# Kernel tuning notes

Measured on AMD Instinct MI355X. Metric: run time of the kernel, lower is better.

The kernel has to match this reference:

```python
import jax, jax.numpy as jnp
import numpy as np

B, S, D, H, T = 64, 512, 768, 384, 22  # batch, seq, bert dim, lstm hidden, tagset+2


def setup_inputs() -> dict:
    key = jax.random.key(0)
    ks = jax.random.split(key, 14)
    hidden_states = jax.random.normal(ks[0], (B, S, D), jnp.float32)
    # strictly increasing wordpiece start offsets, -1 padded (per-sample variable length)
    nw = np.array([S // 2 - (b % 16) * 4 for b in range(B)])  # number of valid start ids
    sid = -np.ones((B, S), np.int64)
    msk = np.zeros((B, S), np.int64)
    for b in range(B):
        sid[b, : nw[b]] = 1 + 2 * np.arange(nw[b])  # max = 2*nw-1 <= S-1
        msk[b, : nw[b] + 1] = 1  # word-level mask: nw+1 words incl. CLS slot
    start_ids = jnp.asarray(sid)
    masks = jnp.asarray(msk)
    sc = 0.05
    h0 = jax.random.normal(ks[1], (2, B, H), jnp.float32)
    c0 = jax.random.normal(ks[2], (2, B, H), jnp.float32)
    W_ih_f = jax.random.normal(ks[3], (4 * H, D), jnp.float32) * sc
    W_hh_f = jax.random.normal(ks[4], (4 * H, H), jnp.float32) * sc
    b_ih_f = jax.random.normal(ks[5], (4 * H,), jnp.float32) * sc
    b_hh_f = jax.random.normal(ks[6], (4 * H,), jnp.float32) * sc
    W_ih_b = jax.random.normal(ks[7], (4 * H, D), jnp.float32) * sc
    W_hh_b = jax.random.normal(ks[8], (4 * H, H), jnp.float32) * sc
    b_ih_b = jax.random.normal(ks[9], (4 * H,), jnp.float32) * sc
    b_hh_b = jax.random.normal(ks[10], (4 * H,), jnp.float32) * sc
    W_lin = jax.random.normal(ks[11], (T, 2 * H), jnp.float32) * sc
    b_lin = jax.random.normal(ks[12], (T,), jnp.float32) * sc
    return {"hidden_states": hidden_states, "h0": h0, "c0": c0,
            "W_ih_f": W_ih_f, "W_hh_f": W_hh_f, "b_ih_f": b_ih_f, "b_hh_f": b_hh_f,
            "W_ih_b": W_ih_b, "W_hh_b": W_hh_b, "b_ih_b": b_ih_b, "b_hh_b": b_hh_b,
            "W_lin": W_lin, "b_lin": b_lin, "start_ids": start_ids, "masks": masks}


def _lstm_dir(x, h0, c0, Wih, Whh, bih, bhh, reverse):
    # x: [B,S,D]; torch gate order i,f,g,o
    xg = jnp.einsum('bsd,gd->bsg', x, Wih) + bih + bhh  # [B,S,4H]
    xs = jnp.swapaxes(xg, 0, 1)  # [S,B,4H]
    if reverse:
        xs = xs[::-1]

    def step(carry, xt):
        h, c = carry
        g = xt + h @ Whh.T
        i, f, gg, o = jnp.split(g, 4, axis=-1)
        c = jax.nn.sigmoid(f) * c + jax.nn.sigmoid(i) * jnp.tanh(gg)
        h = jax.nn.sigmoid(o) * jnp.tanh(c)
        return (h, c), h

    _, hs = jax.lax.scan(step, (h0, c0), xs)
    if reverse:
        hs = hs[::-1]
    return jnp.swapaxes(hs, 0, 1)  # [B,S,H]


def _align(hidden_states, start_ids, masks):
    # word t embedding: t==0 -> token 0 (CLS); 1<=t<n -> token start_ids[t]-1
    # (last wordpiece of word t); t==n -> token start_ids[n-1]; else zero-pad.
    Bb, Ss, _ = hidden_states.shape
    t = jnp.arange(Ss)[None, :]
    valid = start_ids >= 0
    n = valid.sum(-1)  # [B] number of valid start ids
    last_sid = jnp.take_along_axis(start_ids, (n - 1)[:, None], axis=1)  # [B,1]
    idx = jnp.where(t == 0, 0,
          jnp.where(t < n[:, None], start_ids - 1,
          jnp.where(t == n[:, None], last_sid, 0)))
    idx = jnp.clip(idx, 0, Ss - 1)
    gathered = jnp.take_along_axis(hidden_states, idx[:, :, None], axis=1)
    sent_len = masks.sum(-1)  # word-level lengths (second loop in torch code)
    keep = (t < sent_len[:, None])[:, :, None]
    return jnp.where(keep, gathered, 0.0)


def reference(hidden_states, h0, c0, W_ih_f, W_hh_f, b_ih_f, b_hh_f,
              W_ih_b, W_hh_b, b_ih_b, b_hh_b, W_lin, b_lin, start_ids, masks):
    embeds = _align(hidden_states, start_ids, masks)  # q=1,k=0 => wordpiece-only
    hf = _lstm_dir(embeds, h0[0], c0[0], W_ih_f, W_hh_f, b_ih_f, b_hh_f, False)
    hb = _lstm_dir(embeds, h0[1], c0[1], W_ih_b, W_hh_b, b_ih_b, b_hh_b, True)
    lstm_out = jnp.concatenate([hf, hb], axis=-1)  # [B,S,2H]
    # dropout1 is identity in eval mode
    feats = lstm_out @ W_lin.T + b_lin  # [B,S,T]
    return feats
```

## Files before the change

### kernel.cpp

```cpp
#include <hip/hip_runtime.h>

typedef unsigned short u16;
typedef unsigned int u32;
typedef unsigned long long u64;

typedef short bf16x8 __attribute__((ext_vector_type(8)));
typedef float f32x4 __attribute__((ext_vector_type(4)));
typedef u32 u32x4 __attribute__((ext_vector_type(4)));

#define NB 64
#define NS 512
#define ND 768
#define NH 384
#define NT_OUT 22
#define S2 272
#define NG 1536
#define MGEMM (NB*S2)
#define MAGIC 0x5A5AA5A5u
#define MAX_RETRY 1000000

__device__ __forceinline__ u16 f2b(float f) {
    u32 u = __float_as_uint(f);
    u32 r = (u + 0x7fffu + ((u >> 16) & 1u)) >> 16;
    return (u16)r;
}
__device__ __forceinline__ float b2f(u16 s) { return __uint_as_float(((u32)s) << 16); }

__device__ __forceinline__ float sigm(float x) {
    return __builtin_amdgcn_rcpf(1.f + __expf(-x));
}
__device__ __forceinline__ float tanh_(float x) {
    return 1.f - 2.f * __builtin_amdgcn_rcpf(1.f + __expf(2.f * x));
}

__device__ __forceinline__ void gl_lds16(const void* g, void* l) {
    __builtin_amdgcn_global_load_lds(
        (const __attribute__((address_space(1))) unsigned int*)g,
        (__attribute__((address_space(3))) unsigned int*)l, 16, 0, 0);
}

__device__ __forceinline__ u32 ld_sc0(const int* p) {
    u32 v;
    asm volatile("global_load_dword %0, %1, off sc0 nt\n\t"
                 "s_waitcnt vmcnt(0)"
                 : "=&v"(v) : "v"(p) : "memory");
    return v;
}
__device__ __forceinline__ void st_sc0(int* p, u32 v) {
    asm volatile("global_store_dword %0, %1, off sc0" :: "v"(p), "v"(v) : "memory");
}

__device__ __forceinline__ void ld6_fast_nw(const u32* p,
        u32x4& A, u32x4& B, u32x4& C, u32x4& D, u32x4& E, u32x4& F) {
    asm volatile(
        "global_load_dwordx4 %0, %6, off sc0 nt\n\t"
        "global_load_dwordx4 %1, %6, off offset:16 sc0 nt\n\t"
        "global_load_dwordx4 %2, %6, off offset:128 sc0 nt\n\t"
        "global_load_dwordx4 %3, %6, off offset:144 sc0 nt\n\t"
        "global_load_dwordx4 %4, %6, off offset:256 sc0 nt\n\t"
        "global_load_dwordx4 %5, %6, off offset:272 sc0 nt"
        : "=&v"(A), "=&v"(B), "=&v"(C), "=&v"(D), "=&v"(E), "=&v"(F)
        : "v"(p) : "memory");
}
__device__ __forceinline__ void ld6_fast_wt(const u32* p,
        u32x4& A, u32x4& B, u32x4& C, u32x4& D, u32x4& E, u32x4& F) {
    asm volatile(
        "global_load_dwordx4 %0, %6, off sc0 nt\n\t"
        "global_load_dwordx4 %1, %6, off offset:16 sc0 nt\n\t"
        "global_load_dwordx4 %2, %6, off offset:128 sc0 nt\n\t"
        "global_load_dwordx4 %3, %6, off offset:144 sc0 nt\n\t"
        "global_load_dwordx4 %4, %6, off offset:256 sc0 nt\n\t"
        "global_load_dwordx4 %5, %6, off offset:272 sc0 nt\n\t"
        "s_waitcnt vmcnt(0)"
        : "=&v"(A), "=&v"(B), "=&v"(C), "=&v"(D), "=&v"(E), "=&v"(F)
        : "v"(p) : "memory");
}
__device__ __forceinline__ void ld6_slow(const u32* p,
        u32x4& A, u32x4& B, u32x4& C, u32x4& D, u32x4& E, u32x4& F) {
    #pragma unroll
    for (int e = 0; e < 4; e++) {
        A[e] = __hip_atomic_load(p + e,      __ATOMIC_RELAXED, __HIP_MEMORY_SCOPE_AGENT);
        B[e] = __hip_atomic_load(p + 4 + e,  __ATOMIC_RELAXED, __HIP_MEMORY_SCOPE_AGENT);
        C[e] = __hip_atomic_load(p + 32 + e, __ATOMIC_RELAXED, __HIP_MEMORY_SCOPE_AGENT);
        D[e] = __hip_atomic_load(p + 36 + e, __ATOMIC_RELAXED, __HIP_MEMORY_SCOPE_AGENT);
        E[e] = __hip_atomic_load(p + 64 + e, __ATOMIC_RELAXED, __HIP_MEMORY_SCOPE_AGENT);
        F[e] = __hip_atomic_load(p + 68 + e, __ATOMIC_RELAXED, __HIP_MEMORY_SCOPE_AGENT);
    }
}
__device__ __forceinline__ void ld6_nw(bool fast, const u32* p,
        u32x4& A, u32x4& B, u32x4& C, u32x4& D, u32x4& E, u32x4& F) {
    if (fast) ld6_fast_nw(p, A, B, C, D, E, F);
    else      ld6_slow(p, A, B, C, D, E, F);
}
__device__ __forceinline__ void ld6_wt(bool fast, const u32* p,
        u32x4& A, u32x4& B, u32x4& C, u32x4& D, u32x4& E, u32x4& F) {
    if (fast) ld6_fast_wt(p, A, B, C, D, E, F);
    else      ld6_slow(p, A, B, C, D, E, F);
}
__device__ __forceinline__ void st8(bool fast, u32* p, u32x4 lo, u32x4 hi) {
    if (fast)
        asm volatile("global_store_dwordx4 %0, %1, off sc0\n\t"
                     "global_store_dwordx4 %0, %2, off offset:16 sc0"
                     :: "v"(p), "v"(lo), "v"(hi) : "memory");
    else {
        #pragma unroll
        for (int e = 0; e < 4; e++) {
            __hip_atomic_store(p + e,     lo[e], __ATOMIC_RELAXED, __HIP_MEMORY_SCOPE_AGENT);
            __hip_atomic_store(p + 4 + e, hi[e], __ATOMIC_RELAXED, __HIP_MEMORY_SCOPE_AGENT);
        }
    }
}
__device__ __forceinline__ void wait_vm6() {
    __builtin_amdgcn_sched_barrier(0);
    asm volatile("s_waitcnt vmcnt(6)" ::: "memory");
    __builtin_amdgcn_sched_barrier(0);
}
__device__ __forceinline__ void wait_vm0() {
    __builtin_amdgcn_sched_barrier(0);
    asm volatile("s_waitcnt vmcnt(0)" ::: "memory");
    __builtin_amdgcn_sched_barrier(0);
}
__device__ __forceinline__ void ldsbar() {
    asm volatile("s_waitcnt lgkmcnt(0)" ::: "memory");
    __builtin_amdgcn_s_barrier();
    __builtin_amdgcn_sched_barrier(0);
}

__device__ __forceinline__ u32 sum6(const u32x4& a, const u32x4& b, const u32x4& c,
                                    const u32x4& d, const u32x4& e, const u32x4& f) {
    u32 s = (a[0] & 0xffffu) + (a[1] & 0xffffu) + (a[2] & 0xffffu) + (a[3] & 0xffffu);
    s += (b[0] & 0xffffu) + (b[1] & 0xffffu) + (b[2] & 0xffffu) + (b[3] & 0xffffu);
    s += (c[0] & 0xffffu) + (c[1] & 0xffffu) + (c[2] & 0xffffu) + (c[3] & 0xffffu);
    s += (d[0] & 0xffffu) + (d[1] & 0xffffu) + (d[2] & 0xffffu) + (d[3] & 0xffffu);
    s += (e[0] & 0xffffu) + (e[1] & 0xffffu) + (e[2] & 0xffffu) + (e[3] & 0xffffu);
    s += (f[0] & 0xffffu) + (f[1] & 0xffffu) + (f[2] & 0xffffu) + (f[3] & 0xffffu);
    return s;
}
__device__ __forceinline__ bf16x8 packf(const u32x4& lo, const u32x4& hi) {
    union { u32 q[4]; bf16x8 v; } U;
    U.q[0] = __builtin_amdgcn_perm(lo[1], lo[0], 0x07060302u);
    U.q[1] = __builtin_amdgcn_perm(lo[3], lo[2], 0x07060302u);
    U.q[2] = __builtin_amdgcn_perm(hi[1], hi[0], 0x07060302u);
    U.q[3] = __builtin_amdgcn_perm(hi[3], hi[2], 0x07060302u);
    return U.v;
}

__global__ void k_prep(const float* __restrict__ hidden, const int* __restrict__ start_ids,
                       const int* __restrict__ masks, u16* __restrict__ embeds) {
    int b = blockIdx.x >> 2;
    int quarter = blockIdx.x & 3;
    int tid = threadIdx.x;
    __shared__ int red[256];
    int cn = 0, cm = 0;
    for (int s = tid; s < NS; s += 256) {
        cn += (start_ids[b * NS + s] >= 0) ? 1 : 0;
        cm += (masks[b * NS + s] != 0) ? 1 : 0;
    }
    red[tid] = cn + (cm << 16);
    __syncthreads();
    #pragma unroll
    for (int off = 128; off > 0; off >>= 1) {
        if (tid < off) red[tid] += red[tid + off];
        __syncthreads();
    }
    int n = red[0] & 0xffff;
    int slen = red[0] >> 16;
    n = min(max(n, 1), NS);
    int last = start_ids[b * NS + n - 1];
    for (int t = quarter * 68; t < quarter * 68 + 68; ++t) {
        int idx;
        if (t == 0) idx = 0;
        else if (t < n) idx = start_ids[b * NS + t] - 1;
        else if (t == n) idx = last;
        else idx = 0;
        idx = min(max(idx, 0), NS - 1);
        bool keep = t < slen;
        const float* src = hidden + ((size_t)b * NS + idx) * ND;
        u16* dst = embeds + ((size_t)b * S2 + t) * ND;
        if (tid < 192) {
            float4 v = keep ? *(const float4*)(src + tid * 4) : make_float4(0.f, 0.f, 0.f, 0.f);
            union { u16 u[4]; uint2 q; } pk;
            pk.u[0] = f2b(v.x); pk.u[1] = f2b(v.y); pk.u[2] = f2b(v.z); pk.u[3] = f2b(v.w);
            *(uint2*)(dst + tid * 4) = pk.q;
        }
    }
}

__global__ void k_weights(const float* __restrict__ wf, const float* __restrict__ wb,
                          const float* __restrict__ bihf, const float* __restrict__ bhhf,
                          const float* __restrict__ bihb, const float* __restrict__ bhhb,
                          const float* __restrict__ h0,
                          u16* __restrict__ wihcat, float* __restrict__ biascat,
                          u16* __restrict__ h0buf) {
    int i0 = blockIdx.x * blockDim.x + threadIdx.x;
    int NTH = gridDim.x * blockDim.x;
    for (size_t i = i0; i < (size_t)2 * NG * ND; i += NTH) {
        size_t nrow = i / ND, k = i - nrow * ND;
        float v = (nrow < NG) ? wf[nrow * ND + k] : wb[(nrow - NG) * ND + k];
        wihcat[i] = f2b(v);
    }
    for (int i = i0; i < 2 * NG; i += NTH)
        biascat[i] = (i < NG) ? bihf[i] + bhhf[i] : bihb[i - NG] + bhhb[i - NG];
    for (int i = i0; i < 2 * NB * NH; i += NTH) h0buf[i] = f2b(h0[i]);
}

__global__ void k_packwhh(const float* __restrict__ whhf, const float* __restrict__ whhb,
                          u16* __restrict__ pack) {
    int ft = blockIdx.x * 256 + threadIdx.x;
    if (ft >= 2 * 4 * 4 * 6 * 12 * 64) return;
    int lane = ft & 63;
    int grp = ft >> 6;
    int ks = grp % 12; grp /= 12;
    int nt = grp % 6;  grp /= 6;
    int w  = grp & 3;  grp >>= 2;
    int qc = grp & 3;
    int d  = grp >> 2;
    const float* W = d ? whhb : whhf;
    int col = w * NH + qc * 96 + nt * 16 + (lane & 15);
    int k0 = ks * 32 + (lane >> 4) * 8;
    u16* dst = pack + (size_t)ft * 8;
    #pragma unroll
    for (int e = 0; e < 8; e++) dst[e] = f2b(W[(size_t)col * NH + k0 + e]);
}

__launch_bounds__(256, 2)
__global__ void k_gemm(const u16* __restrict__ A, const u16* __restrict__ Bw,
                       const float* __restrict__ biascat, u16* __restrict__ xg) {
    __shared__ u16 As[128 * 32];
    __shared__ u16 Bs[128 * 32];
    int tid = threadIdx.x;
    int lane = tid & 63, wid = tid >> 6;
    int l15 = lane & 15, q4 = lane >> 4;
    int bn = blockIdx.x;
    int bm = blockIdx.y;
    int wm = (wid >> 1) * 64, wn = (wid & 1) * 64;
    f32x4 acc[4][4] = {};
    for (int k0 = 0; k0 < ND; k0 += 32) {
        #pragma unroll
        for (int j = 0; j < 2; j++) {
            int fl = tid + j * 256;
            int row = fl >> 2, cb = fl & 3;
            const u16* ga = A + (size_t)(bm * 128 + row) * ND + k0 + cb * 8;
            gl_lds16(ga, &As[(size_t)(wid * 64 + j * 256) * 8]);
            const u16* gb = Bw + (size_t)(bn * 128 + row) * ND + k0 + cb * 8;
            gl_lds16(gb, &Bs[(size_t)(wid * 64 + j * 256) * 8]);
        }
        __syncthreads();
        bf16x8 af[4], bf[4];
        #pragma unroll
        for (int mt = 0; mt < 4; mt++)
            af[mt] = *(const bf16x8*)&As[(wm + mt * 16 + l15) * 32 + q4 * 8];
        #pragma unroll
        for (int nt = 0; nt < 4; nt++)
            bf[nt] = *(const bf16x8*)&Bs[(wn + nt * 16 + l15) * 32 + q4 * 8];
        #pragma unroll
        for (int mt = 0; mt < 4; mt++)
            #pragma unroll
            for (int nt = 0; nt < 4; nt++)
                acc[mt][nt] = __builtin_amdgcn_mfma_f32_16x16x32_bf16(af[mt], bf[nt], acc[mt][nt], 0, 0, 0);
        __syncthreads();
    }
    #pragma unroll
    for (int nt = 0; nt < 4; nt++) {
        int gn = bn * 128 + wn + nt * 16 + l15;
        int d = gn >= NG ? 1 : 0;
        int col = gn - d * NG;
        float bias = biascat[gn];
        #pragma unroll
        for (int mt = 0; mt < 4; mt++) {
            #pragma unroll
            for (int r = 0; r < 4; r++) {
                int m = bm * 128 + wm + mt * 16 + q4 * 4 + r;
                int b = m / S2, t = m - b * S2;
                float v = acc[mt][nt][r] + bias;
                xg[((size_t)(d * NB + b) * S2 + t) * NG + col] = f2b(v);
            }
        }
    }
}

__launch_bounds__(256, 1)
__global__ void k_recur(const u16* __restrict__ whhpack, const u16* __restrict__ xg,
                        const float* __restrict__ biascat, const u16* __restrict__ h0buf,
                        const float* __restrict__ c0, u16* __restrict__ hout,
                        int* __restrict__ flags, u32* __restrict__ xch) {
    const int blk = blockIdx.x;
    const int qc = blk >> 3;
    const int cl = blk & 7;
    const int d = cl >> 2;
    const int g = cl & 3;
    const int tid = threadIdx.x, lane = tid & 63, w = tid >> 6;
    const int q4 = lane >> 4, l15 = lane & 15;

    __shared__ float preact[4][16 * 96];
    __shared__ u16 hlds[16 * 104];
    __shared__ int s_fast;

    bf16x8 bfr[6][12];
    #pragma unroll
    for (int nt = 0; nt < 6; nt++)
        #pragma unroll
        for (int j = 0; j < 12; j++) {
            int ksg = ((qc + (j / 3)) & 3) * 3 + (j % 3);
            bfr[nt][j] = *(const bf16x8*)(whhpack +
                ((size_t)((((d * 4 + qc) * 4 + w) * 6 + nt) * 12 + ksg) * 64 + lane) * 8);
        }

    const int bb = tid / 12;
    const int j0 = (tid % 12) * 8;
    float cre[8];
    if (tid < 192) {
        const float* cp = c0 + (size_t)(d * NB + g * 16 + bb) * NH + qc * 96 + j0;
        #pragma unroll
        for (int e = 0; e < 8; e++) cre[e] = cp[e];
    }
    float biasreg[6];
    #pragma unroll
    for (int nt = 0; nt < 6; nt++)
        biasreg[nt] = biascat[d * NG + w * NH + qc * 96 + nt * 16 + l15];

    if (tid == 0) {
        int* pzb = flags + cl * 64;
        int* pmb = flags + 2048 + cl * 64;
        st_sc0(pzb + qc * 16, MAGIC);
        u32 seen = 1u << qc;
        for (int spin = 0; spin < 512 && seen != 0xFu; ++spin) {
            #pragma unroll
            for (int r = 0; r < 4; ++r)
                if (!((seen >> r) & 1u) && ld_sc0(pzb + r * 16) == MAGIC) seen |= 1u << r;
            __builtin_amdgcn_s_sleep(2);
        }
        __hip_atomic_store(pmb + qc * 16, (int)(0x100u | seen),
                           __ATOMIC_RELAXED, __HIP_MEMORY_SCOPE_AGENT);
        u32 m = 0xFu;
        int spin2 = 0;
        #pragma unroll
        for (int r = 0; r < 4; ++r) {
            u32 v;
            do {
                v = (u32)__hip_atomic_load(pmb + r * 16, __ATOMIC_RELAXED,
                                           __HIP_MEMORY_SCOPE_AGENT);
            } while (!(v & 0x100u) && ++spin2 < MAX_RETRY);
            m &= v;
        }
        s_fast = ((m & 0xFu) == 0xFu && spin2 < MAX_RETRY) ? 1 : 0;
    }
    __syncthreads();
    const bool fast = (s_fast != 0);

    const u16* xgd = xg + (size_t)d * NB * S2 * NG;

    float ci[6][4];
    auto preload = [&](int it2) {
        int s2 = d ? (NS - 1 - it2) : it2;
        if (s2 < S2) {
            const u16* xrow = xgd + ((size_t)(g * 16) * S2 + s2) * NG + w * NH + qc * 96 + l15;
            #pragma unroll
            for (int nt = 0; nt < 6; nt++)
                #pragma unroll
                for (int r = 0; r < 4; r++)
                    ci[nt][r] = b2f(xrow[(size_t)(q4 * 4 + r) * S2 * NG + nt * 16]);
        } else {
            #pragma unroll
            for (int nt = 0; nt < 6; nt++)
                #pragma unroll
                for (int r = 0; r < 4; r++) ci[nt][r] = biasreg[nt];
        }
    };
    preload(0);

    #pragma unroll 1
    for (int it = 0; it < NS; ++it) {
        int s = d ? (NS - 1 - it) : it;
        f32x4 acc[6];

        if (it == 0) {
            bf16x8 af0[12];
            const u16* hp = h0buf + (size_t)(d * NB + g * 16) * NH;
            #pragma unroll
            for (int j = 0; j < 12; j++) {
                int ksg = ((qc + (j / 3)) & 3) * 3 + (j % 3);
                af0[j] = *(const bf16x8*)(hp + (size_t)l15 * NH + ksg * 32 + q4 * 8);
            }
            #pragma unroll
            for (int nt = 0; nt < 6; nt++) {
                acc[nt][0] = ci[nt][0]; acc[nt][1] = ci[nt][1];
                acc[nt][2] = ci[nt][2]; acc[nt][3] = ci[nt][3];
            }
            preload(1);
            #pragma unroll
            for (int j = 0; j < 12; j++)
                #pragma unroll
                for (int nt = 0; nt < 6; nt++)
                    acc[nt] = __builtin_amdgcn_mfma_f32_16x16x32_bf16(af0[j], bfr[nt][j], acc[nt], 0, 0, 0);
        } else {
            bf16x8 afo0 = *(const bf16x8*)&hlds[l15 * 104 + 0 * 32 + q4 * 8];
            bf16x8 afo1 = *(const bf16x8*)&hlds[l15 * 104 + 1 * 32 + q4 * 8];
            bf16x8 afo2 = *(const bf16x8*)&hlds[l15 * 104 + 2 * 32 + q4 * 8];
            const u32 T = (u32)it;
            const u32 want = T * 24u;
            u32* xrow = xch + (((size_t)(T & 3u) * 8 + cl) * 16 + l15) * 384 + q4 * 8;
            u32* pA = xrow + ((qc + 1) & 3) * 96;
            u32* pB = xrow + ((qc + 2) & 3) * 96;
            u32* pC = xrow + ((qc + 3) & 3) * 96;
            u32x4 a0, a1, a2, a3, a4, a5, b0, b1, b2, b3, b4, b5, e0, e1, e2, e3, e4, e5;
            ld6_nw(fast, pA, a0, a1, a2, a3, a4, a5);
            ld6_nw(fast, pB, b0, b1, b2, b3, b4, b5);
            #pragma unroll
            for (int nt = 0; nt < 6; nt++) {
                acc[nt][0] = ci[nt][0]; acc[nt][1] = ci[nt][1];
                acc[nt][2] = ci[nt][2]; acc[nt][3] = ci[nt][3];
            }
            #pragma unroll
            for (int nt = 0; nt < 6; nt++)
                acc[nt] = __builtin_amdgcn_mfma_f32_16x16x32_bf16(afo0, bfr[nt][0], acc[nt], 0, 0, 0);
            #pragma unroll
            for (int nt = 0; nt < 6; nt++)
                acc[nt] = __builtin_amdgcn_mfma_f32_16x16x32_bf16(afo1, bfr[nt][1], acc[nt], 0, 0, 0);
            #pragma unroll
            for (int nt = 0; nt < 6; nt++)
                acc[nt] = __builtin_amdgcn_mfma_f32_16x16x32_bf16(afo2, bfr[nt][2], acc[nt], 0, 0, 0);
            wait_vm6();
            int tries = 0;
            while (!__all(sum6(a0, a1, a2, a3, a4, a5) == want) && ++tries < MAX_RETRY)
                ld6_wt(fast, pA, a0, a1, a2, a3, a4, a5);
            bf16x8 afA0 = packf(a0, a1), afA1 = packf(a2, a3), afA2 = packf(a4, a5);
            ld6_nw(fast, pC, e0, e1, e2, e3, e4, e5);
            #pragma unroll
            for (int nt = 0; nt < 6; nt++)
                acc[nt] = __builtin_amdgcn_mfma_f32_16x16x32_bf16(afA0, bfr[nt][3], acc[nt], 0, 0, 0);
            #pragma unroll
            for (int nt = 0; nt < 6; nt++)
                acc[nt] = __builtin_amdgcn_mfma_f32_16x16x32_bf16(afA1, bfr[nt][4], acc[nt], 0, 0, 0);
            #pragma unroll
            for (int nt = 0; nt < 6; nt++)
                acc[nt] = __builtin_amdgcn_mfma_f32_16x16x32_bf16(afA2, bfr[nt][5], acc[nt], 0, 0, 0);
            wait_vm6();
            tries = 0;
            while (!__all(sum6(b0, b1, b2, b3, b4, b5) == want) && ++tries < MAX_RETRY)
                ld6_wt(fast, pB, b0, b1, b2, b3, b4, b5);
            bf16x8 afB0 = packf(b0, b1), afB1 = packf(b2, b3), afB2 = packf(b4, b5);
            #pragma unroll
            for (int nt = 0; nt < 6; nt++)
                acc[nt] = __builtin_amdgcn_mfma_f32_16x16x32_bf16(afB0, bfr[nt][6], acc[nt], 0, 0, 0);
            #pragma unroll
            for (int nt = 0; nt < 6; nt++)
                acc[nt] = __builtin_amdgcn_mfma_f32_16x16x32_bf16(afB1, bfr[nt][7], acc[nt], 0, 0, 0);
            #pragma unroll
            for (int nt = 0; nt < 6; nt++)
                acc[nt] = __builtin_amdgcn_mfma_f32_16x16x32_bf16(afB2, bfr[nt][8], acc[nt], 0, 0, 0);
            wait_vm0();
            tries = 0;
            while (!__all(sum6(e0, e1, e2, e3, e4, e5) == want) && ++tries < MAX_RETRY)
                ld6_wt(fast, pC, e0, e1, e2, e3, e4, e5);
            bf16x8 afC0 = packf(e0, e1), afC1 = packf(e2, e3), afC2 = packf(e4, e5);
            if (it + 1 < NS) preload(it + 1);
            #pragma unroll
            for (int nt = 0; nt < 6; nt++)
                acc[nt] = __builtin_amdgcn_mfma_f32_16x16x32_bf16(afC0, bfr[nt][9], acc[nt], 0, 0, 0);
            #pragma unroll
            for (int nt = 0; nt < 6; nt++)
                acc[nt] = __builtin_amdgcn_mfma_f32_16x16x32_bf16(afC1, bfr[nt][10], acc[nt], 0, 0, 0);
            #pragma unroll
            for (int nt = 0; nt < 6; nt++)
                acc[nt] = __builtin_amdgcn_mfma_f32_16x16x32_bf16(afC2, bfr[nt][11], acc[nt], 0, 0, 0);
        }

        #pragma unroll
        for (int nt = 0; nt < 6; nt++)
            #pragma unroll
            for (int r = 0; r < 4; r++)
                preact[w][(q4 * 4 + r) * 96 + nt * 16 + l15] = acc[nt][r];
        ldsbar();

        if (tid < 192) {
            int idx = bb * 96 + j0;
            u16* ho = hout + (((size_t)(d * NB + g * 16 + bb)) * NS + s) * NH + qc * 96 + j0;
            union { u16 u[8]; u32x4 v4; } pk;
            #pragma unroll
            for (int e = 0; e < 8; e++) {
                float gi = preact[0][idx + e], gf = preact[1][idx + e];
                float gg = preact[2][idx + e], go = preact[3][idx + e];
                float c = cre[e];
                float cn = sigm(gf) * c + sigm(gi) * tanh_(gg);
                float hn = sigm(go) * tanh_(cn);
                cre[e] = cn;
                pk.u[e] = f2b(hn);
            }
            u32 t2 = (u32)it + 1u;
            u32x4 lo, hi;
            lo[0] = ((u32)pk.u[0] << 16) | t2; lo[1] = ((u32)pk.u[1] << 16) | t2;
            lo[2] = ((u32)pk.u[2] << 16) | t2; lo[3] = ((u32)pk.u[3] << 16) | t2;
            hi[0] = ((u32)pk.u[4] << 16) | t2; hi[1] = ((u32)pk.u[5] << 16) | t2;
            hi[2] = ((u32)pk.u[6] << 16) | t2; hi[3] = ((u32)pk.u[7] << 16) | t2;
            u32* xp = xch + (((size_t)(t2 & 3u) * 8 + cl) * 16 + bb) * 384 + qc * 96 + j0;
            st8(fast, xp, lo, hi);
            *(u32x4*)ho = pk.v4;
            *(u32x4*)&hlds[bb * 104 + j0] = pk.v4;
        }
        wait_vm0();
        ldsbar();
    }
}

__global__ void k_final(const u16* __restrict__ hout, const float* __restrict__ wlin,
                        const float* __restrict__ blin, float* __restrict__ out) {
    int r = blockIdx.x * 256 + threadIdx.x;
    int b = r >> 9, t = r & 511;
    const u16* hf = hout + ((size_t)b * NS + t) * NH;
    const u16* hb = hout + ((size_t)(NB + b) * NS + t) * NH;
    float acc[NT_OUT];
    #pragma unroll
    for (int tt = 0; tt < NT_OUT; tt++) acc[tt] = blin[tt];
    #pragma unroll 1
    for (int half = 0; half < 2; half++) {
        const u16* hp = half ? hb : hf;
        #pragma unroll 1
        for (int k8 = 0; k8 < NH / 8; k8++) {
            uint4 pk = *(const uint4*)(hp + k8 * 8);
            float x[8];
            x[0] = __uint_as_float(pk.x << 16); x[1] = __uint_as_float(pk.x & 0xffff0000u);
            x[2] = __uint_as_float(pk.y << 16); x[3] = __uint_as_float(pk.y & 0xffff0000u);
            x[4] = __uint_as_float(pk.z << 16); x[5] = __uint_as_float(pk.z & 0xffff0000u);
            x[6] = __uint_as_float(pk.w << 16); x[7] = __uint_as_float(pk.w & 0xffff0000u);
            int kk = half * NH + k8 * 8;
            #pragma unroll
            for (int e = 0; e < 8; e++)
                #pragma unroll
                for (int tt = 0; tt < NT_OUT; tt++)
                    acc[tt] += x[e] * wlin[tt * (2 * NH) + kk + e];
        }
    }
    float* op = out + (size_t)r * NT_OUT;
    #pragma unroll
    for (int tt = 0; tt < NT_OUT; tt++) op[tt] = acc[tt];
}

extern "C" void kernel_launch(void* const* d_in, const int* in_sizes, int n_in,
                              void* d_out, int out_size, void* d_ws, size_t ws_size,
                              hipStream_t stream) {
    const float* hidden = (const float*)d_in[0];
    const float* h0     = (const float*)d_in[1];
    const float* c0     = (const float*)d_in[2];
    const float* Wihf   = (const float*)d_in[3];
    const float* Whhf   = (const float*)d_in[4];
    const float* bihf   = (const float*)d_in[5];
    const float* bhhf   = (const float*)d_in[6];
    const float* Wihb   = (const float*)d_in[7];
    const float* Whhb   = (const float*)d_in[8];
    const float* bihb   = (const float*)d_in[9];
    const float* bhhb   = (const float*)d_in[10];
    const float* Wlin   = (const float*)d_in[11];
    const float* blin   = (const float*)d_in[12];
    const int* start_ids = (const int*)d_in[13];
    const int* masks     = (const int*)d_in[14];
    float* out = (float*)d_out;

    char* ws = (char*)d_ws;
    size_t off = 0;
    auto alloc = [&](size_t bytes) { void* p = ws + off; off += (bytes + 255) & ~(size_t)255; return p; };
    u16* embeds   = (u16*)alloc((size_t)MGEMM * ND * 2);
    u16* wihcat   = (u16*)alloc((size_t)2 * NG * ND * 2);
    float* biascat = (float*)alloc((size_t)2 * NG * 4);
    u16* whhpack  = (u16*)alloc((size_t)2 * NG * NH * 2);
    u16* h0buf    = (u16*)alloc((size_t)2 * NB * NH * 2);
    u16* xg       = (u16*)alloc((size_t)2 * NB * S2 * NG * 2);
    u16* hout     = (u16*)alloc((size_t)2 * NB * NS * NH * 2);
    int* flags    = (int*)alloc((size_t)8 * NS * 4);
    u32* xch      = (u32*)alloc((size_t)4 * 8 * 16 * 384 * 4);

    (void)hipMemsetAsync(flags, 0, (size_t)8 * NS * 4, stream);
    (void)hipMemsetAsync(xch, 0, (size_t)4 * 8 * 16 * 384 * 4, stream);
    k_prep<<<256, 256, 0, stream>>>(hidden, start_ids, masks, embeds);
    k_weights<<<512, 256, 0, stream>>>(Wihf, Wihb, bihf, bhhf, bihb, bhhb, h0,
                                       wihcat, biascat, h0buf);
    k_packwhh<<<576, 256, 0, stream>>>(Whhf, Whhb, whhpack);
    dim3 ggrid(2 * NG / 128, MGEMM / 128);
    k_gemm<<<ggrid, 256, 0, stream>>>(embeds, wihcat, biascat, xg);
    k_recur<<<32, 256, 0, stream>>>(whhpack, xg, biascat, h0buf, c0, hout, flags, xch);
    k_final<<<128, 256, 0, stream>>>(hout, Wlin, blin, out);
}
```

Baseline: 2.657 ms.

## Issue all exchange loads up front and prefetch x-gates with counted waits

Reworks the per-step schedule of the recurrent LSTM kernel. All three peer h-exchange loads are now issued at the start of each step, and the next step's x-gate preload uses inline asm ushort loads that are drained with explicit vmcnt counts instead of full waits. The end-of-step vmcnt(0) wait is removed and the preact LDS row stride is padded from 96 to 100 to reduce bank conflicts. This shortens the serialized latency chain per timestep, but relies on exact vmcnt accounting, which is fragile: the slow path issues per-element atomic loads that may not match the assumed counts.

```diff
diff --git a/kernel.cpp b/kernel.cpp
--- a/kernel.cpp
+++ b/kernel.cpp
@@ -110,16 +110,9 @@
         }
     }
 }
-__device__ __forceinline__ void wait_vm6() {
-    __builtin_amdgcn_sched_barrier(0);
-    asm volatile("s_waitcnt vmcnt(6)" ::: "memory");
-    __builtin_amdgcn_sched_barrier(0);
-}
-__device__ __forceinline__ void wait_vm0() {
-    __builtin_amdgcn_sched_barrier(0);
-    asm volatile("s_waitcnt vmcnt(0)" ::: "memory");
-    __builtin_amdgcn_sched_barrier(0);
-}
+#define WAIT_VM(N) do { __builtin_amdgcn_sched_barrier(0); \
+    asm volatile("s_waitcnt vmcnt(" #N ")" ::: "memory"); \
+    __builtin_amdgcn_sched_barrier(0); } while (0)
 __device__ __forceinline__ void ldsbar() {
     asm volatile("s_waitcnt lgkmcnt(0)" ::: "memory");
     __builtin_amdgcn_s_barrier();
@@ -292,7 +285,7 @@
     const int tid = threadIdx.x, lane = tid & 63, w = tid >> 6;
     const int q4 = lane >> 4, l15 = lane & 15;
 
-    __shared__ float preact[4][16 * 96];
+    __shared__ float preact[4][16 * 100];
     __shared__ u16 hlds[16 * 104];
     __shared__ int s_fast;
 
@@ -350,24 +343,29 @@
 
     const u16* xgd = xg + (size_t)d * NB * S2 * NG;
 
-    float ci[6][4];
-    auto preload = [&](int it2) {
+    u32 cr[6][4];
+    auto issue_preload = [&](int it2) -> bool {
         int s2 = d ? (NS - 1 - it2) : it2;
-        if (s2 < S2) {
-            const u16* xrow = xgd + ((size_t)(g * 16) * S2 + s2) * NG + w * NH + qc * 96 + l15;
-            #pragma unroll
-            for (int nt = 0; nt < 6; nt++)
-                #pragma unroll
-                for (int r = 0; r < 4; r++)
-                    ci[nt][r] = b2f(xrow[(size_t)(q4 * 4 + r) * S2 * NG + nt * 16]);
-        } else {
-            #pragma unroll
-            for (int nt = 0; nt < 6; nt++)
-                #pragma unroll
-                for (int r = 0; r < 4; r++) ci[nt][r] = biasreg[nt];
-        }
+        bool ok = (s2 >= 0) && (s2 < S2);
+        int s2c = min(max(s2, 0), S2 - 1);
+        const u16* rp = xgd + ((size_t)(g * 16) * S2 + s2c) * NG + w * NH + qc * 96 + l15;
+        #pragma unroll
+        for (int r = 0; r < 4; r++) {
+            const u16* base = rp + (size_t)(q4 * 4 + r) * S2 * NG;
+            asm volatile(
+                "global_load_ushort %0, %6, off\n\t"
+                "global_load_ushort %1, %6, off offset:32\n\t"
+                "global_load_ushort %2, %6, off offset:64\n\t"
+                "global_load_ushort %3, %6, off offset:96\n\t"
+                "global_load_ushort %4, %6, off offset:128\n\t"
+                "global_load_ushort %5, %6, off offset:160"
+                : "=&v"(cr[0][r]), "=&v"(cr[1][r]), "=&v"(cr[2][r]),
+                  "=&v"(cr[3][r]), "=&v"(cr[4][r]), "=&v"(cr[5][r])
+                : "v"(base) : "memory");
+        }
+        return ok;
     };
-    preload(0);
+    bool vld = issue_preload(0);
 
     #pragma unroll 1
     for (int it = 0; it < NS; ++it) {
@@ -375,28 +373,23 @@
         f32x4 acc[6];
 
         if (it == 0) {
-            bf16x8 af0[12];
+            WAIT_VM(0);
+            #pragma unroll
+            for (int nt = 0; nt < 6; nt++)
+                #pragma unroll
+                for (int r = 0; r < 4; r++)
+                    acc[nt][r] = vld ? __uint_as_float(cr[nt][r] << 16) : biasreg[nt];
+            vld = issue_preload(1);
             const u16* hp = h0buf + (size_t)(d * NB + g * 16) * NH;
             #pragma unroll
             for (int j = 0; j < 12; j++) {
                 int ksg = ((qc + (j / 3)) & 3) * 3 + (j % 3);
-                af0[j] = *(const bf16x8*)(hp + (size_t)l15 * NH + ksg * 32 + q4 * 8);
+                bf16x8 af = *(const bf16x8*)(hp + (size_t)l15 * NH + ksg * 32 + q4 * 8);
+                #pragma unroll
+                for (int nt = 0; nt < 6; nt++)
+                    acc[nt] = __builtin_amdgcn_mfma_f32_16x16x32_bf16(af, bfr[nt][j], acc[nt], 0, 0, 0);
             }
-            #pragma unroll
-            for (int nt = 0; nt < 6; nt++) {
-                acc[nt][0] = ci[nt][0]; acc[nt][1] = ci[nt][1];
-                acc[nt][2] = ci[nt][2]; acc[nt][3] = ci[nt][3];
-            }
-            preload(1);
-            #pragma unroll
-            for (int j = 0; j < 12; j++)
-                #pragma unroll
-                for (int nt = 0; nt < 6; nt++)
-                    acc[nt] = __builtin_amdgcn_mfma_f32_16x16x32_bf16(af0[j], bfr[nt][j], acc[nt], 0, 0, 0);
         } else {
-            bf16x8 afo0 = *(const bf16x8*)&hlds[l15 * 104 + 0 * 32 + q4 * 8];
-            bf16x8 afo1 = *(const bf16x8*)&hlds[l15 * 104 + 1 * 32 + q4 * 8];
-            bf16x8 afo2 = *(const bf16x8*)&hlds[l15 * 104 + 2 * 32 + q4 * 8];
             const u32 T = (u32)it;
             const u32 want = T * 24u;
             u32* xrow = xch + (((size_t)(T & 3u) * 8 + cl) * 16 + l15) * 384 + q4 * 8;
@@ -406,11 +399,17 @@
             u32x4 a0, a1, a2, a3, a4, a5, b0, b1, b2, b3, b4, b5, e0, e1, e2, e3, e4, e5;
             ld6_nw(fast, pA, a0, a1, a2, a3, a4, a5);
             ld6_nw(fast, pB, b0, b1, b2, b3, b4, b5);
-            #pragma unroll
-            for (int nt = 0; nt < 6; nt++) {
-                acc[nt][0] = ci[nt][0]; acc[nt][1] = ci[nt][1];
-                acc[nt][2] = ci[nt][2]; acc[nt][3] = ci[nt][3];
-            }
+            ld6_nw(fast, pC, e0, e1, e2, e3, e4, e5);
+            WAIT_VM(18);
+            #pragma unroll
+            for (int nt = 0; nt < 6; nt++)
+                #pragma unroll
+                for (int r = 0; r < 4; r++)
+                    acc[nt][r] = vld ? __uint_as_float(cr[nt][r] << 16) : biasreg[nt];
+            vld = issue_preload(it + 1);
+            bf16x8 afo0 = *(const bf16x8*)&hlds[l15 * 104 + 0 * 32 + q4 * 8];
+            bf16x8 afo1 = *(const bf16x8*)&hlds[l15 * 104 + 1 * 32 + q4 * 8];
+            bf16x8 afo2 = *(const bf16x8*)&hlds[l15 * 104 + 2 * 32 + q4 * 8];
             #pragma unroll
             for (int nt = 0; nt < 6; nt++)
                 acc[nt] = __builtin_amdgcn_mfma_f32_16x16x32_bf16(afo0, bfr[nt][0], acc[nt], 0, 0, 0);
@@ -420,61 +419,66 @@
             #pragma unroll
             for (int nt = 0; nt < 6; nt++)
                 acc[nt] = __builtin_amdgcn_mfma_f32_16x16x32_bf16(afo2, bfr[nt][2], acc[nt], 0, 0, 0);
-            wait_vm6();
-            int tries = 0;
+            int tries;
+            WAIT_VM(36);
+            tries = 0;
             while (!__all(sum6(a0, a1, a2, a3, a4, a5) == want) && ++tries < MAX_RETRY)
                 ld6_wt(fast, pA, a0, a1, a2, a3, a4, a5);
-            bf16x8 afA0 = packf(a0, a1), afA1 = packf(a2, a3), afA2 = packf(a4, a5);
-            ld6_nw(fast, pC, e0, e1, e2, e3, e4, e5);
-            #pragma unroll
-            for (int nt = 0; nt < 6; nt++)
-                acc[nt] = __builtin_amdgcn_mfma_f32_16x16x32_bf16(afA0, bfr[nt][3], acc[nt], 0, 0, 0);
-            #pragma unroll
-            for (int nt = 0; nt < 6; nt++)
-                acc[nt] = __builtin_amdgcn_mfma_f32_16x16x32_bf16(afA1, bfr[nt][4], acc[nt], 0, 0, 0);
-            #pragma unroll
-            for (int nt = 0; nt < 6; nt++)
-                acc[nt] = __builtin_amdgcn_mfma_f32_16x16x32_bf16(afA2, bfr[nt][5], acc[nt], 0, 0, 0);
-            wait_vm6();
+            {
+                bf16x8 fA0 = packf(a0, a1), fA1 = packf(a2, a3), fA2 = packf(a4, a5);
+                #pragma unroll
+                for (int nt = 0; nt < 6; nt++)
+                    acc[nt] = __builtin_amdgcn_mfma_f32_16x16x32_bf16(fA0, bfr[nt][3], acc[nt], 0, 0, 0);
+                #pragma unroll
+                for (int nt = 0; nt < 6; nt++)
+                    acc[nt] = __builtin_amdgcn_mfma_f32_16x16x32_bf16(fA1, bfr[nt][4], acc[nt], 0, 0, 0);
+                #pragma unroll
+                for (int nt = 0; nt < 6; nt++)
+                    acc[nt] = __builtin_amdgcn_mfma_f32_16x16x32_bf16(fA2, bfr[nt][5], acc[nt], 0, 0, 0);
+            }
+            WAIT_VM(30);
             tries = 0;
             while (!__all(sum6(b0, b1, b2, b3, b4, b5) == want) && ++tries < MAX_RETRY)
                 ld6_wt(fast, pB, b0, b1, b2, b3, b4, b5);
-            bf16x8 afB0 = packf(b0, b1), afB1 = packf(b2, b3), afB2 = packf(b4, b5);
-            #pragma unroll
-            for (int nt = 0; nt < 6; nt++)
-                acc[nt] = __builtin_amdgcn_mfma_f32_16x16x32_bf16(afB0, bfr[nt][6], acc[nt], 0, 0, 0);
-            #pragma unroll
-            for (int nt = 0; nt < 6; nt++)
-                acc[nt] = __builtin_amdgcn_mfma_f32_16x16x32_bf16(afB1, bfr[nt][7], acc[nt], 0, 0, 0);
-            #pragma unroll
-            for (int nt = 0; nt < 6; nt++)
-                acc[nt] = __builtin_amdgcn_mfma_f32_16x16x32_bf16(afB2, bfr[nt][8], acc[nt], 0, 0, 0);
-            wait_vm0();
+            {
+                bf16x8 fB0 = packf(b0, b1), fB1 = packf(b2, b3), fB2 = packf(b4, b5);
+                #pragma unroll
+                for (int nt = 0; nt < 6; nt++)
+                    acc[nt] = __builtin_amdgcn_mfma_f32_16x16x32_bf16(fB0, bfr[nt][6], acc[nt], 0, 0, 0);
+                #pragma unroll
+                for (int nt = 0; nt < 6; nt++)
+                    acc[nt] = __builtin_amdgcn_mfma_f32_16x16x32_bf16(fB1, bfr[nt][7], acc[nt], 0, 0, 0);
+                #pragma unroll
+                for (int nt = 0; nt < 6; nt++)
+                    acc[nt] = __builtin_amdgcn_mfma_f32_16x16x32_bf16(fB2, bfr[nt][8], acc[nt], 0, 0, 0);
+            }
+            WAIT_VM(24);
             tries = 0;
             while (!__all(sum6(e0, e1, e2, e3, e4, e5) == want) && ++tries < MAX_RETRY)
                 ld6_wt(fast, pC, e0, e1, e2, e3, e4, e5);
-            bf16x8 afC0 = packf(e0, e1), afC1 = packf(e2, e3), afC2 = packf(e4, e5);
-            if (it + 1 < NS) preload(it + 1);
-            #pragma unroll
-            for (int nt = 0; nt < 6; nt++)
-                acc[nt] = __builtin_amdgcn_mfma_f32_16x16x32_bf16(afC0, bfr[nt][9], acc[nt], 0, 0, 0);
-            #pragma unroll
-            for (int nt = 0; nt < 6; nt++)
-                acc[nt] = __builtin_amdgcn_mfma_f32_16x16x32_bf16(afC1, bfr[nt][10], acc[nt], 0, 0, 0);
-            #pragma unroll
-            for (int nt = 0; nt < 6; nt++)
-                acc[nt] = __builtin_amdgcn_mfma_f32_16x16x32_bf16(afC2, bfr[nt][11], acc[nt], 0, 0, 0);
+            {
+                bf16x8 fC0 = packf(e0, e1), fC1 = packf(e2, e3), fC2 = packf(e4, e5);
+                #pragma unroll
+                for (int nt = 0; nt < 6; nt++)
+                    acc[nt] = __builtin_amdgcn_mfma_f32_16x16x32_bf16(fC0, bfr[nt][9], acc[nt], 0, 0, 0);
+                #pragma unroll
+                for (int nt = 0; nt < 6; nt++)
+                    acc[nt] = __builtin_amdgcn_mfma_f32_16x16x32_bf16(fC1, bfr[nt][10], acc[nt], 0, 0, 0);
+                #pragma unroll
+                for (int nt = 0; nt < 6; nt++)
+                    acc[nt] = __builtin_amdgcn_mfma_f32_16x16x32_bf16(fC2, bfr[nt][11], acc[nt], 0, 0, 0);
+            }
         }
 
         #pragma unroll
         for (int nt = 0; nt < 6; nt++)
             #pragma unroll
             for (int r = 0; r < 4; r++)
-                preact[w][(q4 * 4 + r) * 96 + nt * 16 + l15] = acc[nt][r];
+                preact[w][(q4 * 4 + r) * 100 + nt * 16 + l15] = acc[nt][r];
         ldsbar();
 
         if (tid < 192) {
-            int idx = bb * 96 + j0;
+            int idx = bb * 100 + j0;
             u16* ho = hout + (((size_t)(d * NB + g * 16 + bb)) * NS + s) * NH + qc * 96 + j0;
             union { u16 u[8]; u32x4 v4; } pk;
             #pragma unroll
@@ -498,7 +502,6 @@
             *(u32x4*)ho = pk.v4;
             *(u32x4*)&hlds[bb * 104 + j0] = pk.v4;
         }
-        wait_vm0();
         ldsbar();
     }
 }
```

Result: slower. 2.895 ms (+8.9%).
